# Kernel optimization log

Hardware: AMD Instinct MI355X
Metric: run time of the kernel (lower is better)

Reference implementation:

```python
import jax, jax.numpy as jnp
import numpy as np

N_EXP = 8
TOP_K = 2


def setup_inputs() -> dict:
    key = jax.random.key(0)
    k0, k1, k2, k3 = jax.random.split(key, 4)
    B, T, D = 2, 2048, 1024
    H = 4 * D
    s = 0.02
    x = jax.random.normal(k0, (B, T, D), jnp.float32)
    wg = (jax.random.normal(k1, (D, N_EXP), jnp.float32) * s)       # router gate (no bias)
    w1 = (jax.random.normal(k2, (N_EXP, D, H), jnp.float32) * s)    # expert c_fc weights
    b1 = jnp.zeros((N_EXP, H), jnp.float32)
    w2 = (jax.random.normal(k3, (N_EXP, H, D), jnp.float32) * s)    # expert c_proj weights
    b2 = jnp.zeros((N_EXP, D), jnp.float32)
    return {"x": x, "wg": wg, "w1": w1, "b1": b1, "w2": w2, "b2": b2}


def reference(x, wg, w1, b1, w2, b2):
    B, T, D = x.shape
    xt = x.reshape(B * T, D)                                  # (batch token) embed
    logits = xt @ wg                                          # [BT, E]
    probs = jax.nn.softmax(logits.astype(jnp.float32), axis=-1)
    _topw, topi = jax.lax.top_k(probs, TOP_K)                 # topi: [BT, K] selected experts
    # Grouped-GEMM over all experts (dense form of the per-expert gather-MLP-scatter)
    h = jax.nn.gelu(jnp.einsum('td,edh->eth', xt, w1) + b1[:, None, :], approximate=False)
    out_all = jnp.einsum('eth,ehd->etd', h, w2) + b2[:, None, :]   # [E, BT, D]
    t_idx = jnp.arange(B * T)
    final = jnp.zeros_like(xt)
    for j in range(TOP_K):
        # Bug-faithful to the source: the loop weights each selected expert's output
        # by weights_exps[top_x, idx_exp] where idx_exp is the SLOT index (0..K-1),
        # i.e. the softmax prob of expert column j -- not the top-k weight.
        final = final + out_all[topi[:, j], t_idx] * probs[:, j][:, None].astype(xt.dtype)
    return final.reshape(B, T, D), logits
```

## Files before the change

kernel.cpp:

```cpp
#include <hip/hip_runtime.h>
#include <hip/hip_bf16.h>
#include <math.h>
#include <stdint.h>

#define BT  4096
#define DIM 1024
#define HID 4096
#define NE  8
#define TMX 72

typedef __attribute__((ext_vector_type(8))) short short8v;
typedef __attribute__((ext_vector_type(4))) float f32x4;
typedef unsigned short ushort_t;

typedef __attribute__((address_space(1))) const void gas_void;
typedef __attribute__((address_space(3))) void las_void;
#define GLOAD_LDS16(g, l) __builtin_amdgcn_global_load_lds((gas_void*)(g), (las_void*)(l), 16, 0, 0)

__device__ inline ushort_t f2bf(float f) {
  __hip_bfloat16 b = __float2bfloat16(f);
  union { __hip_bfloat16 h; ushort_t u; } cv;
  cv.h = b;
  return cv.u;
}

__global__ __launch_bounds__(256) void k_prep_router(
    const float* __restrict__ x, const float* __restrict__ wg,
    ushort_t* __restrict__ xbf, float* __restrict__ logits_out,
    float* __restrict__ probs01, int* __restrict__ assign,
    int* __restrict__ cur) {
  int t = blockIdx.x;
  int tid = threadIdx.x;
  const float* xr = x + (size_t)t * DIM;
  float4 v = ((const float4*)xr)[tid];
  ushort4 o;
  o.x = f2bf(v.x); o.y = f2bf(v.y); o.z = f2bf(v.z); o.w = f2bf(v.w);
  ((ushort4*)(xbf + (size_t)t * DIM))[tid] = o;

  float vv[4] = {v.x, v.y, v.z, v.w};
  float part[NE];
#pragma unroll
  for (int e = 0; e < NE; e++) part[e] = 0.f;
#pragma unroll
  for (int i = 0; i < 4; i++) {
    const float4* wr = (const float4*)(wg + (size_t)(tid * 4 + i) * NE);
    float4 a = wr[0], b = wr[1];
    part[0] += vv[i] * a.x; part[1] += vv[i] * a.y;
    part[2] += vv[i] * a.z; part[3] += vv[i] * a.w;
    part[4] += vv[i] * b.x; part[5] += vv[i] * b.y;
    part[6] += vv[i] * b.z; part[7] += vv[i] * b.w;
  }
#pragma unroll
  for (int e = 0; e < NE; e++)
    for (int off = 32; off > 0; off >>= 1)
      part[e] += __shfl_xor(part[e], off);

  __shared__ float red[4][NE];
  int lane = tid & 63, wv = tid >> 6;
  if (lane == 0) {
#pragma unroll
    for (int e = 0; e < NE; e++) red[wv][e] = part[e];
  }
  __syncthreads();
  if (tid == 0) {
    float s8[NE];
#pragma unroll
    for (int e = 0; e < NE; e++)
      s8[e] = red[0][e] + red[1][e] + red[2][e] + red[3][e];
    float m = s8[0];
    for (int e = 1; e < NE; e++) m = fmaxf(m, s8[e]);
    float p[NE], s = 0.f;
    for (int e = 0; e < NE; e++) { p[e] = expf(s8[e] - m); s += p[e]; }
    float inv = 1.f / s;
    for (int e = 0; e < NE; e++) p[e] *= inv;
    for (int e = 0; e < NE; e++) logits_out[(size_t)t * NE + e] = s8[e];
    probs01[t * 2 + 0] = p[0];
    probs01[t * 2 + 1] = p[1];
    int b0 = 0;
    for (int e = 1; e < NE; e++) if (p[e] > p[b0]) b0 = e;
    int b1 = (b0 == 0) ? 1 : 0;
    for (int e = 0; e < NE; e++) if (e != b0 && p[e] > p[b1]) b1 = e;
    int pos0 = atomicAdd(&cur[b0], 1);
    assign[b0 * BT + pos0] = t * 2 + 0;
    int pos1 = atomicAdd(&cur[b1], 1);
    assign[b1 * BT + pos1] = t * 2 + 1;
  }
}

__global__ __launch_bounds__(256) void k_transpose(const float* __restrict__ src,
                                                   ushort_t* __restrict__ dst,
                                                   int R, int C,
                                                   int* __restrict__ cur) {
  if (cur && blockIdx.x == 0 && blockIdx.y == 0 && blockIdx.z == 0 &&
      threadIdx.x < NE)
    cur[threadIdx.x] = 0;
  __shared__ float tile[64][65];
  int e = blockIdx.z;
  const float* s = src + (size_t)e * R * C;
  ushort_t* d = dst + (size_t)e * R * C;
  int c0 = blockIdx.x * 64, r0 = blockIdx.y * 64;
  int t = threadIdx.x;
  int lr = t >> 4;
  int lc4 = (t & 15) * 4;
#pragma unroll
  for (int i = 0; i < 4; i++) {
    int r = lr + 16 * i;
    float4 v = *(const float4*)&s[(size_t)(r0 + r) * C + c0 + lc4];
    tile[r][lc4 + 0] = v.x; tile[r][lc4 + 1] = v.y;
    tile[r][lc4 + 2] = v.z; tile[r][lc4 + 3] = v.w;
  }
  __syncthreads();
  int c = t >> 3, r8 = (t & 7) * 8;
#pragma unroll
  for (int p = 0; p < 2; p++) {
    int cc = c + 32 * p;
    short8v ov;
#pragma unroll
    for (int i = 0; i < 8; i++) ov[i] = (short)f2bf(tile[r8 + i][cc]);
    *(short8v*)&d[(size_t)(c0 + cc) * R + r0 + r8] = ov;
  }
}

__global__ void k_plan(const int* __restrict__ cur, int* __restrict__ segoff,
                       int* __restrict__ blk_e, int* __restrict__ blk_m0) {
  if (threadIdx.x == 0 && blockIdx.x == 0) {
    int s = 0;
    for (int e = 0; e < NE; e++) { segoff[e] = s; s += cur[e]; }
    int t = 0;
    for (int e = 0; e < NE; e++) {
      int mb = (cur[e] + 127) >> 7;
      for (int i = 0; i < mb; i++) { blk_e[t] = e; blk_m0[t] = i << 7; t++; }
    }
    for (; t < TMX; t++) { blk_e[t] = -1; blk_m0[t] = 0; }
  }
}

#define VM2 asm volatile("s_waitcnt vmcnt(2)" ::: "memory")
#define VM0 asm volatile("s_waitcnt vmcnt(0)" ::: "memory")
#define VMN do {} while (0)

#define TILEK(TB, T, VMX, DOSTG)                                                \
  { short8v bv[2], af[4];                                                       \
    _Pragma("unroll")                                                           \
    for (int n = 0; n < 2; n++)                                                 \
      bv[n] = *(const short8v*)&Bv[TB][wn * 32 + n * 16 + lr][xsw];             \
    _Pragma("unroll")                                                           \
    for (int m = 0; m < 4; m++)                                                 \
      af[m] = *(const short8v*)&A[TB][wm * 64 + m * 16 + lr][xsw];              \
    if (DOSTG) { STAGE((((TB) + 2) % 3), ((T) + 2) * 32); }                     \
    VMX;                                                                        \
    __builtin_amdgcn_s_barrier();                                               \
    __builtin_amdgcn_sched_barrier(0);                                          \
    __builtin_amdgcn_s_setprio(1);                                              \
    _Pragma("unroll")                                                           \
    for (int m = 0; m < 4; m++)                                                 \
      _Pragma("unroll")                                                         \
      for (int n = 0; n < 2; n++)                                               \
        acc[m][n] = __builtin_amdgcn_mfma_f32_16x16x32_bf16(af[m], bv[n],       \
                                                            acc[m][n], 0, 0, 0);\
    __builtin_amdgcn_s_setprio(0); }

__global__ __launch_bounds__(512, 6) void k_gemm1(
    const ushort_t* __restrict__ xbf, const ushort_t* __restrict__ wt1,
    const float* __restrict__ b1,
    const int* __restrict__ assign, const int* __restrict__ cur,
    const int* __restrict__ segoff, const int* __restrict__ blk_e,
    const int* __restrict__ blk_m0, ushort_t* __restrict__ hbuf) {
  const int nwg = 32 * TMX;
  int f = blockIdx.x;
  int lg = (f & 7) * (nwg >> 3) + (f >> 3);
  int m_idx = lg % TMX;
  int n_idx = lg / TMX;
  int e = blk_e[m_idx];
  if (e < 0) return;
  int m0 = blk_m0[m_idx];
  int count = cur[e];
  int n0 = n_idx << 7;

  __shared__ __attribute__((aligned(16))) ushort_t A[3][128][32];
  __shared__ __attribute__((aligned(16))) ushort_t Bv[3][128][32];
  int tid = threadIdx.x;
  int lane = tid & 63, wid = tid >> 6;

  int srow = lane >> 2;
  int sunit = ((lane & 3) ^ ((lane >> 3) & 3)) << 3;
  int pA0 = m0 + wid * 16 + srow;
  int tok0 = (pA0 < count) ? (assign[e * BT + pA0] >> 1) : 0;
  const ushort_t* gA0 = xbf + (size_t)tok0 * DIM + sunit;
  const ushort_t* gB0 = wt1 + ((size_t)e * HID + n0 + wid * 16 + srow) * DIM + sunit;

  int wm = wid >> 2, wn = wid & 3;
  int lr = lane & 15, g = lane >> 4;
  int xsw = ((g ^ ((lr >> 1) & 3)) << 3);
  f32x4 acc[4][2];
  f32x4 zero = {0.f, 0.f, 0.f, 0.f};
#pragma unroll
  for (int m = 0; m < 4; m++)
#pragma unroll
    for (int n = 0; n < 2; n++) acc[m][n] = zero;

#define STAGE(SL, K0)                                          \
  { GLOAD_LDS16(gA0 + (K0), &A[SL][wid * 16][0]);              \
    GLOAD_LDS16(gB0 + (K0), &Bv[SL][wid * 16][0]); }

  STAGE(0, 0);
  STAGE(1, 32);
  VM2;
  __builtin_amdgcn_s_barrier();
  __builtin_amdgcn_sched_barrier(0);

  const int NT = DIM / 32;
  for (int t = 0; t < NT - 2; t += 3) {
    TILEK(0, t + 0, VM2, 1);
    TILEK(1, t + 1, VM2, 1);
    TILEK(2, t + 2, VM2, 1);
  }
  TILEK(0, NT - 2, VM0, 0);
  TILEK(1, NT - 1, VMN, 0);
#undef STAGE

  int so = segoff[e];
#pragma unroll
  for (int m = 0; m < 4; m++) {
#pragma unroll
    for (int j = 0; j < 4; j++) {
      int p = m0 + wm * 64 + m * 16 + g * 4 + j;
      if (p >= count) continue;
      ushort_t* hr = hbuf + (size_t)(so + p) * HID;
#pragma unroll
      for (int n = 0; n < 2; n++) {
        int col = n0 + wn * 32 + n * 16 + lr;
        float v = acc[m][n][j] + b1[e * HID + col];
        float gl = 0.5f * v * (1.0f + erff(v * 0.70710678118654752f));
        hr[col] = f2bf(gl);
      }
    }
  }
}

__global__ __launch_bounds__(512, 6) void k_gemm2(
    const ushort_t* __restrict__ hbuf, const ushort_t* __restrict__ wt2,
    const float* __restrict__ b2,
    const int* __restrict__ assign, const int* __restrict__ cur,
    const int* __restrict__ segoff, const int* __restrict__ blk_e,
    const int* __restrict__ blk_m0, float* __restrict__ contrib) {
  const int nwg = 8 * TMX;
  int f = blockIdx.x;
  int lg = (f & 7) * (nwg >> 3) + (f >> 3);
  int m_idx = lg % TMX;
  int n_idx = lg / TMX;
  int e = blk_e[m_idx];
  if (e < 0) return;
  int m0 = blk_m0[m_idx];
  int count = cur[e];
  int n0 = n_idx << 7;
  int so = segoff[e];

  __shared__ __attribute__((aligned(16))) ushort_t A[3][128][32];
  __shared__ __attribute__((aligned(16))) ushort_t Bv[3][128][32];
  int tid = threadIdx.x;
  int lane = tid & 63, wid = tid >> 6;

  int srow = lane >> 2;
  int sunit = ((lane & 3) ^ ((lane >> 3) & 3)) << 3;
  int pA0 = m0 + wid * 16 + srow;
  int pa0 = (pA0 < count) ? pA0 : (count - 1);
  const ushort_t* gA0 = hbuf + (size_t)(so + pa0) * HID + sunit;
  const ushort_t* gB0 = wt2 + ((size_t)e * DIM + n0 + wid * 16 + srow) * HID + sunit;

  int wm = wid >> 2, wn = wid & 3;
  int lr = lane & 15, g = lane >> 4;
  int xsw = ((g ^ ((lr >> 1) & 3)) << 3);
  f32x4 acc[4][2];
  f32x4 zero = {0.f, 0.f, 0.f, 0.f};
#pragma unroll
  for (int m = 0; m < 4; m++)
#pragma unroll
    for (int n = 0; n < 2; n++) acc[m][n] = zero;

#define STAGE(SL, K0)                                          \
  { GLOAD_LDS16(gA0 + (K0), &A[SL][wid * 16][0]);              \
    GLOAD_LDS16(gB0 + (K0), &Bv[SL][wid * 16][0]); }

  STAGE(0, 0);
  STAGE(1, 32);
  VM2;
  __builtin_amdgcn_s_barrier();
  __builtin_amdgcn_sched_barrier(0);

  const int NT = HID / 32;
  for (int t = 0; t < NT - 2; t += 3) {
    TILEK(0, t + 0, VM2, 1);
    TILEK(1, t + 1, VM2, 1);
    TILEK(2, t + 2, VM2, 1);
  }
  TILEK(0, NT - 2, VM0, 0);
  TILEK(1, NT - 1, VMN, 0);
#undef STAGE

#pragma unroll
  for (int m = 0; m < 4; m++) {
#pragma unroll
    for (int j = 0; j < 4; j++) {
      int p = m0 + wm * 64 + m * 16 + g * 4 + j;
      if (p >= count) continue;
      int a = assign[e * BT + p];
      int t = a >> 1, slot = a & 1;
      float* cr = contrib + ((size_t)slot * BT + t) * DIM;
#pragma unroll
      for (int n = 0; n < 2; n++) {
        int col = n0 + wn * 32 + n * 16 + lr;
        cr[col] = acc[m][n][j] + b2[e * DIM + col];
      }
    }
  }
}

__global__ void k_combine(const float* __restrict__ contrib,
                          const float* __restrict__ probs01,
                          float* __restrict__ out) {
  int idx = blockIdx.x * blockDim.x + threadIdx.x;
  const int n4 = BT * DIM / 4;
  if (idx >= n4) return;
  int t = idx >> 8;
  float wA = probs01[t * 2 + 0], wB = probs01[t * 2 + 1];
  float4 c0 = ((const float4*)contrib)[idx];
  float4 c1 = ((const float4*)(contrib + (size_t)BT * DIM))[idx];
  float4 o;
  o.x = c0.x * wA + c1.x * wB;
  o.y = c0.y * wA + c1.y * wB;
  o.z = c0.z * wA + c1.z * wB;
  o.w = c0.w * wA + c1.w * wB;
  ((float4*)out)[idx] = o;
}

extern "C" void kernel_launch(void* const* d_in, const int* in_sizes, int n_in,
                              void* d_out, int out_size, void* d_ws, size_t ws_size,
                              hipStream_t stream) {
  const float* x  = (const float*)d_in[0];
  const float* wg = (const float*)d_in[1];
  const float* w1 = (const float*)d_in[2];
  const float* b1 = (const float*)d_in[3];
  const float* w2 = (const float*)d_in[4];
  const float* b2 = (const float*)d_in[5];
  float* out = (float*)d_out;
  float* logits_out = out + (size_t)BT * DIM;

  char* ws = (char*)d_ws;
  size_t off = 0;
  auto alloc = [&](size_t bytes) -> void* {
    void* p = ws + off;
    off = (off + bytes + 255) & ~(size_t)255;
    return p;
  };
  ushort_t* xbf    = (ushort_t*)alloc((size_t)BT * DIM * 2);
  ushort_t* wt1    = (ushort_t*)alloc((size_t)NE * HID * DIM * 2);
  ushort_t* wt2    = (ushort_t*)alloc((size_t)NE * DIM * HID * 2);
  ushort_t* hbuf   = (ushort_t*)alloc((size_t)2 * BT * HID * 2);
  float*    contrib= (float*)alloc((size_t)2 * BT * DIM * 4);
  float*    probs01= (float*)alloc((size_t)BT * 2 * 4);
  int*      assign = (int*)alloc((size_t)NE * BT * 4);
  int*      cur    = (int*)alloc(64);
  int*      segoff = (int*)alloc(64);
  int*      blk_e  = (int*)alloc(TMX * 4);
  int*      blk_m0 = (int*)alloc(TMX * 4);
  if (off > ws_size) return;

  hipLaunchKernelGGL(k_transpose, dim3(HID / 64, DIM / 64, NE), dim3(256), 0, stream,
                     w1, wt1, DIM, HID, cur);
  hipLaunchKernelGGL(k_transpose, dim3(DIM / 64, HID / 64, NE), dim3(256), 0, stream,
                     w2, wt2, HID, DIM, (int*)nullptr);
  hipLaunchKernelGGL(k_prep_router, dim3(BT), dim3(256), 0, stream,
                     x, wg, xbf, logits_out, probs01, assign, cur);
  hipLaunchKernelGGL(k_plan, dim3(1), dim3(64), 0, stream, cur, segoff,
                     blk_e, blk_m0);
  hipLaunchKernelGGL(k_gemm1, dim3(32 * TMX), dim3(512), 0, stream,
                     xbf, wt1, b1, assign, cur, segoff, blk_e, blk_m0, hbuf);
  hipLaunchKernelGGL(k_gemm2, dim3(8 * TMX), dim3(512), 0, stream,
                     hbuf, wt2, b2, assign, cur, segoff, blk_e, blk_m0, contrib);
  hipLaunchKernelGGL(k_combine, dim3((BT * DIM / 4 + 255) / 256), dim3(256), 0, stream,
                     contrib, probs01, out);
}
```

Measured before the change: 441.1 us.

## Fuse weight transposes with router prepass and switch GEMMs to double buffering

Merges the two weight-transpose kernels and the router kernel into a single launch, dispatching by block index, and resets the expert counters with a memset instead of from inside the first transpose. Both grouped GEMMs drop from a three-stage to a two-stage LDS pipeline that waits for all outstanding loads each K-step, and their launch bounds are raised from 6 to 8 for more occupancy. Launch overhead and LDS footprint go down, but each tile now waits for its loads immediately, so less global-load latency is hidden.

```diff
diff --git a/kernel.cpp b/kernel.cpp
--- a/kernel.cpp
+++ b/kernel.cpp
@@ -24,12 +24,55 @@
   return cv.u;
 }
 
-__global__ __launch_bounds__(256) void k_prep_router(
+__device__ __forceinline__ void transpose_body(
+    const float* __restrict__ src, ushort_t* __restrict__ dst,
+    int R, int C, int bx, int by, int e, float (*tile)[65]) {
+  const float* s = src + (size_t)e * R * C;
+  ushort_t* d = dst + (size_t)e * R * C;
+  int c0 = bx * 64, r0 = by * 64;
+  int t = threadIdx.x;
+  int lr = t >> 4;
+  int lc4 = (t & 15) * 4;
+#pragma unroll
+  for (int i = 0; i < 4; i++) {
+    int r = lr + 16 * i;
+    float4 v = *(const float4*)&s[(size_t)(r0 + r) * C + c0 + lc4];
+    tile[r][lc4 + 0] = v.x; tile[r][lc4 + 1] = v.y;
+    tile[r][lc4 + 2] = v.z; tile[r][lc4 + 3] = v.w;
+  }
+  __syncthreads();
+  int c = t >> 3, r8 = (t & 7) * 8;
+#pragma unroll
+  for (int p = 0; p < 2; p++) {
+    int cc = c + 32 * p;
+    short8v ov;
+#pragma unroll
+    for (int i = 0; i < 8; i++) ov[i] = (short)f2bf(tile[r8 + i][cc]);
+    *(short8v*)&d[(size_t)(c0 + cc) * R + r0 + r8] = ov;
+  }
+}
+
+__global__ __launch_bounds__(256) void k_prepass(
     const float* __restrict__ x, const float* __restrict__ wg,
     ushort_t* __restrict__ xbf, float* __restrict__ logits_out,
     float* __restrict__ probs01, int* __restrict__ assign,
-    int* __restrict__ cur) {
-  int t = blockIdx.x;
+    int* __restrict__ cur,
+    const float* __restrict__ w1, ushort_t* __restrict__ wt1,
+    const float* __restrict__ w2, ushort_t* __restrict__ wt2) {
+  __shared__ __attribute__((aligned(16))) float tile[64][65];
+  int id = blockIdx.x;
+  if (id < 8192) {
+    int bx = id & 63, by = (id >> 6) & 15, bz = id >> 10;
+    transpose_body(w1, wt1, DIM, HID, bx, by, bz, tile);
+    return;
+  }
+  if (id < 16384) {
+    int t = id - 8192;
+    int bx = t & 15, by = (t >> 4) & 63, bz = t >> 10;
+    transpose_body(w2, wt2, HID, DIM, bx, by, bz, tile);
+    return;
+  }
+  int t = id - 16384;
   int tid = threadIdx.x;
   const float* xr = x + (size_t)t * DIM;
   float4 v = ((const float4*)xr)[tid];
@@ -55,7 +98,7 @@
     for (int off = 32; off > 0; off >>= 1)
       part[e] += __shfl_xor(part[e], off);
 
-  __shared__ float red[4][NE];
+  float (*red)[NE] = (float(*)[NE])tile;
   int lane = tid & 63, wv = tid >> 6;
   if (lane == 0) {
 #pragma unroll
@@ -87,40 +130,6 @@
   }
 }
 
-__global__ __launch_bounds__(256) void k_transpose(const float* __restrict__ src,
-                                                   ushort_t* __restrict__ dst,
-                                                   int R, int C,
-                                                   int* __restrict__ cur) {
-  if (cur && blockIdx.x == 0 && blockIdx.y == 0 && blockIdx.z == 0 &&
-      threadIdx.x < NE)
-    cur[threadIdx.x] = 0;
-  __shared__ float tile[64][65];
-  int e = blockIdx.z;
-  const float* s = src + (size_t)e * R * C;
-  ushort_t* d = dst + (size_t)e * R * C;
-  int c0 = blockIdx.x * 64, r0 = blockIdx.y * 64;
-  int t = threadIdx.x;
-  int lr = t >> 4;
-  int lc4 = (t & 15) * 4;
-#pragma unroll
-  for (int i = 0; i < 4; i++) {
-    int r = lr + 16 * i;
-    float4 v = *(const float4*)&s[(size_t)(r0 + r) * C + c0 + lc4];
-    tile[r][lc4 + 0] = v.x; tile[r][lc4 + 1] = v.y;
-    tile[r][lc4 + 2] = v.z; tile[r][lc4 + 3] = v.w;
-  }
-  __syncthreads();
-  int c = t >> 3, r8 = (t & 7) * 8;
-#pragma unroll
-  for (int p = 0; p < 2; p++) {
-    int cc = c + 32 * p;
-    short8v ov;
-#pragma unroll
-    for (int i = 0; i < 8; i++) ov[i] = (short)f2bf(tile[r8 + i][cc]);
-    *(short8v*)&d[(size_t)(c0 + cc) * R + r0 + r8] = ov;
-  }
-}
-
 __global__ void k_plan(const int* __restrict__ cur, int* __restrict__ segoff,
                        int* __restrict__ blk_e, int* __restrict__ blk_m0) {
   if (threadIdx.x == 0 && blockIdx.x == 0) {
@@ -135,7 +144,6 @@
   }
 }
 
-#define VM2 asm volatile("s_waitcnt vmcnt(2)" ::: "memory")
 #define VM0 asm volatile("s_waitcnt vmcnt(0)" ::: "memory")
 #define VMN do {} while (0)
 
@@ -147,7 +155,7 @@
     _Pragma("unroll")                                                           \
     for (int m = 0; m < 4; m++)                                                 \
       af[m] = *(const short8v*)&A[TB][wm * 64 + m * 16 + lr][xsw];              \
-    if (DOSTG) { STAGE((((TB) + 2) % 3), ((T) + 2) * 32); }                     \
+    if (DOSTG) { STAGE(((TB) ^ 1), ((T) + 1) * 32); }                           \
     VMX;                                                                        \
     __builtin_amdgcn_s_barrier();                                               \
     __builtin_amdgcn_sched_barrier(0);                                          \
@@ -160,7 +168,7 @@
                                                             acc[m][n], 0, 0, 0);\
     __builtin_amdgcn_s_setprio(0); }
 
-__global__ __launch_bounds__(512, 6) void k_gemm1(
+__global__ __launch_bounds__(512, 8) void k_gemm1(
     const ushort_t* __restrict__ xbf, const ushort_t* __restrict__ wt1,
     const float* __restrict__ b1,
     const int* __restrict__ assign, const int* __restrict__ cur,
@@ -177,8 +185,8 @@
   int count = cur[e];
   int n0 = n_idx << 7;
 
-  __shared__ __attribute__((aligned(16))) ushort_t A[3][128][32];
-  __shared__ __attribute__((aligned(16))) ushort_t Bv[3][128][32];
+  __shared__ __attribute__((aligned(16))) ushort_t A[2][128][32];
+  __shared__ __attribute__((aligned(16))) ushort_t Bv[2][128][32];
   int tid = threadIdx.x;
   int lane = tid & 63, wid = tid >> 6;
 
@@ -204,18 +212,16 @@
     GLOAD_LDS16(gB0 + (K0), &Bv[SL][wid * 16][0]); }
 
   STAGE(0, 0);
-  STAGE(1, 32);
-  VM2;
+  VM0;
   __builtin_amdgcn_s_barrier();
   __builtin_amdgcn_sched_barrier(0);
 
   const int NT = DIM / 32;
-  for (int t = 0; t < NT - 2; t += 3) {
-    TILEK(0, t + 0, VM2, 1);
-    TILEK(1, t + 1, VM2, 1);
-    TILEK(2, t + 2, VM2, 1);
-  }
-  TILEK(0, NT - 2, VM0, 0);
+  for (int t = 0; t < NT - 2; t += 2) {
+    TILEK(0, t + 0, VM0, 1);
+    TILEK(1, t + 1, VM0, 1);
+  }
+  TILEK(0, NT - 2, VM0, 1);
   TILEK(1, NT - 1, VMN, 0);
 #undef STAGE
 
@@ -238,7 +244,7 @@
   }
 }
 
-__global__ __launch_bounds__(512, 6) void k_gemm2(
+__global__ __launch_bounds__(512, 8) void k_gemm2(
     const ushort_t* __restrict__ hbuf, const ushort_t* __restrict__ wt2,
     const float* __restrict__ b2,
     const int* __restrict__ assign, const int* __restrict__ cur,
@@ -256,8 +262,8 @@
   int n0 = n_idx << 7;
   int so = segoff[e];
 
-  __shared__ __attribute__((aligned(16))) ushort_t A[3][128][32];
-  __shared__ __attribute__((aligned(16))) ushort_t Bv[3][128][32];
+  __shared__ __attribute__((aligned(16))) ushort_t A[2][128][32];
+  __shared__ __attribute__((aligned(16))) ushort_t Bv[2][128][32];
   int tid = threadIdx.x;
   int lane = tid & 63, wid = tid >> 6;
 
@@ -283,18 +289,16 @@
     GLOAD_LDS16(gB0 + (K0), &Bv[SL][wid * 16][0]); }
 
   STAGE(0, 0);
-  STAGE(1, 32);
-  VM2;
+  VM0;
   __builtin_amdgcn_s_barrier();
   __builtin_amdgcn_sched_barrier(0);
 
   const int NT = HID / 32;
-  for (int t = 0; t < NT - 2; t += 3) {
-    TILEK(0, t + 0, VM2, 1);
-    TILEK(1, t + 1, VM2, 1);
-    TILEK(2, t + 2, VM2, 1);
-  }
-  TILEK(0, NT - 2, VM0, 0);
+  for (int t = 0; t < NT - 2; t += 2) {
+    TILEK(0, t + 0, VM0, 1);
+    TILEK(1, t + 1, VM0, 1);
+  }
+  TILEK(0, NT - 2, VM0, 1);
   TILEK(1, NT - 1, VMN, 0);
 #undef STAGE
 
@@ -366,12 +370,10 @@
   int*      blk_m0 = (int*)alloc(TMX * 4);
   if (off > ws_size) return;
 
-  hipLaunchKernelGGL(k_transpose, dim3(HID / 64, DIM / 64, NE), dim3(256), 0, stream,
-                     w1, wt1, DIM, HID, cur);
-  hipLaunchKernelGGL(k_transpose, dim3(DIM / 64, HID / 64, NE), dim3(256), 0, stream,
-                     w2, wt2, HID, DIM, (int*)nullptr);
-  hipLaunchKernelGGL(k_prep_router, dim3(BT), dim3(256), 0, stream,
-                     x, wg, xbf, logits_out, probs01, assign, cur);
+  hipMemsetAsync(cur, 0, NE * sizeof(int), stream);
+  hipLaunchKernelGGL(k_prepass, dim3(16384 + BT), dim3(256), 0, stream,
+                     x, wg, xbf, logits_out, probs01, assign, cur,
+                     w1, wt1, w2, wt2);
   hipLaunchKernelGGL(k_plan, dim3(1), dim3(64), 0, stream, cur, segoff,
                      blk_e, blk_m0);
   hipLaunchKernelGGL(k_gemm1, dim3(32 * TMX), dim3(512), 0, stream,
```

New measurement: 662.1 us. 50.1% more time.
